# Performance work log

Measured on AMD Instinct MI355X. Metric: run time of the kernel, lower is better.

## Reference

```python
import jax, jax.numpy as jnp
import numpy as np

N_NODES = 100000
N_EDGES = 1600000
D = 64


def setup_inputs() -> dict:
    key = jax.random.key(0)
    k1, k2, k3, k4 = jax.random.split(key, 4)
    x = jax.random.normal(k1, (N_NODES, D), dtype=jnp.float32)
    # glorot-uniform scale for Linear weight [out_dim, in_dim]
    stdv = np.sqrt(6.0 / (D + D)).astype(np.float32)
    W = jax.random.uniform(k2, (D, D), dtype=jnp.float32, minval=-stdv, maxval=stdv)
    bias = jnp.zeros((D,), dtype=jnp.float32)  # forward() uses a zero bias
    edge_index = jax.random.randint(k3, (2, N_EDGES), 0, N_NODES, dtype=jnp.int64)
    counts = jax.random.randint(k4, (N_NODES,), 0, 16, dtype=jnp.int64)
    out_edge_index = jnp.arange(N_EDGES, dtype=jnp.int64)
    return {"x": x, "W": W, "bias": bias, "edge_index": edge_index,
            "counts": counts, "out_edge_index": out_edge_index, "layer_i": 0}


def reference(x, W, bias, edge_index, counts, out_edge_index, layer_i):
    # GCN layer: y = x @ W^T; gather by source; scatter-sum by destination; add bias.
    # counts / out_edge_index / layer_i are layout hints for the fused CUDA kernel
    # (mygraph.gcn) and do not change the math.
    y = x @ W.T                              # [N, D_out]
    src = edge_index[0]                      # [E]
    dst = edge_index[1]                      # [E]
    msgs = y[src]                            # [E, D_out] edge gather
    out = jax.ops.segment_sum(msgs, dst, num_segments=x.shape[0])  # [N, D_out]
    return out + bias
```

## Files before the change

### kernel.cpp

```cpp
#include <hip/hip_runtime.h>


#define DIM 64
#define BN 64
#define BN_SHIFT 6
#define BN_MASK 63
#define NB_MAX 2048
#define PB 256
#define KMAX 8
#define CAPE 1536
#define OVF_MAX 262144
#define AGS 72

typedef __attribute__((ext_vector_type(8))) short short8;
typedef __attribute__((ext_vector_type(4))) float f32x4;

__device__ __forceinline__ unsigned short f32_to_bf16_rne(float f) {
    unsigned u = __float_as_uint(f);
    unsigned r = u + 0x7FFFu + ((u >> 16) & 1u);
    return (unsigned short)(r >> 16);
}

__device__ __forceinline__ void pk2(float a, float b, unsigned &ph, unsigned &pl) {
    unsigned ha = f32_to_bf16_rne(a);
    unsigned hb = f32_to_bf16_rne(b);
    ph = ha | (hb << 16);
    float fa = __uint_as_float(ha << 16);
    float fb = __uint_as_float(hb << 16);
    unsigned la = f32_to_bf16_rne(a - fa);
    unsigned lb = f32_to_bf16_rne(b - fb);
    pl = la | (lb << 16);
}

__device__ __forceinline__ f32x4 mfma16(uint4 a, uint4 b, f32x4 c) {
    return __builtin_amdgcn_mfma_f32_16x16x32_bf16(
        __builtin_bit_cast(short8, a), __builtin_bit_cast(short8, b), c, 0, 0, 0);
}

__global__ __launch_bounds__(1024) void fused_prep_reg_kernel(
        const float* __restrict__ x, const int* __restrict__ ei,
        ushort4* __restrict__ xb4, int* __restrict__ gcnt,
        int* __restrict__ binned, int* __restrict__ ovf,
        int* __restrict__ ovfcnt, int E, int N, int nb, int total4) {
    __shared__ int h[NB_MAX];
    const int t = threadIdx.x;
    const int bid = blockIdx.x;

    for (int b = t; b < nb; b += 1024) h[b] = 0;
    __syncthreads();

    int es[KMAX], ds[KMAX];
    #pragma unroll
    for (int k = 0; k < KMAX; ++k) {
        int e = (k * PB + bid) * 1024 + t;
        if (e < E) {
            es[k] = ei[e];
            ds[k] = ei[E + e];
            atomicAdd(&h[ds[k] >> BN_SHIFT], 1);
        } else {
            ds[k] = -1;
        }
    }

    for (int i = bid * 1024 + t; i < total4; i += PB * 1024) {
        float4 v = ((const float4*)x)[i];
        ushort4 o;
        o.x = f32_to_bf16_rne(v.x); o.y = f32_to_bf16_rne(v.y);
        o.z = f32_to_bf16_rne(v.z); o.w = f32_to_bf16_rne(v.w);
        xb4[i] = o;
    }
    if (bid == 0 && t < 16) {
        ushort4 z; z.x = 0; z.y = 0; z.z = 0; z.w = 0;
        xb4[(size_t)N * 16 + t] = z;
    }
    __syncthreads();

    for (int b = t; b < nb; b += 1024) {
        int c = h[b];
        int base = (c > 0) ? atomicAdd(&gcnt[b], c) : 0;
        h[b] = b * CAPE + base;
    }
    __syncthreads();

    #pragma unroll
    for (int k = 0; k < KMAX; ++k) {
        if (ds[k] >= 0) {
            int b = ds[k] >> BN_SHIFT;
            int p = atomicAdd(&h[b], 1);
            if (p < b * CAPE + CAPE) {
                binned[p] = (es[k] << BN_SHIFT) | (ds[k] & BN_MASK);
            } else {
                int q = atomicAdd(ovfcnt, 1);
                if (q < OVF_MAX) { ovf[2 * q] = es[k]; ovf[2 * q + 1] = ds[k]; }
            }
        }
    }
}

__global__ __launch_bounds__(1024) void fused_prep_kernel(
        const float* __restrict__ x, const int* __restrict__ ei,
        ushort4* __restrict__ xb4, int* __restrict__ gcnt,
        int* __restrict__ binned, int* __restrict__ ovf,
        int* __restrict__ ovfcnt, int E, int N, int nb, int total4) {
    __shared__ int h[NB_MAX];
    const int t = threadIdx.x;
    const int bid = blockIdx.x;

    for (int b = t; b < nb; b += 1024) h[b] = 0;
    __syncthreads();

    for (int i = bid * 1024 + t; i < total4; i += PB * 1024) {
        float4 v = ((const float4*)x)[i];
        ushort4 o;
        o.x = f32_to_bf16_rne(v.x); o.y = f32_to_bf16_rne(v.y);
        o.z = f32_to_bf16_rne(v.z); o.w = f32_to_bf16_rne(v.w);
        xb4[i] = o;
    }
    if (bid == 0 && t < 16) {
        ushort4 z; z.x = 0; z.y = 0; z.z = 0; z.w = 0;
        xb4[(size_t)N * 16 + t] = z;
    }

    for (int e = bid * 1024 + t; e < E; e += PB * 1024)
        atomicAdd(&h[ei[E + e] >> BN_SHIFT], 1);
    __syncthreads();

    for (int b = t; b < nb; b += 1024) {
        int c = h[b];
        int base = (c > 0) ? atomicAdd(&gcnt[b], c) : 0;
        h[b] = b * CAPE + base;
    }
    __syncthreads();

    for (int e = bid * 1024 + t; e < E; e += PB * 1024) {
        int s = ei[e];
        int d = ei[E + e];
        int b = d >> BN_SHIFT;
        int p = atomicAdd(&h[b], 1);
        if (p < b * CAPE + CAPE) {
            binned[p] = (s << BN_SHIFT) | (d & BN_MASK);
        } else {
            int q = atomicAdd(ovfcnt, 1);
            if (q < OVF_MAX) { ovf[2 * q] = s; ovf[2 * q + 1] = d; }
        }
    }
}

__device__ __forceinline__ void acc8(float (&a)[8], const uint4& v) {
    a[0] += __uint_as_float(v.x << 16); a[1] += __uint_as_float(v.x & 0xFFFF0000u);
    a[2] += __uint_as_float(v.y << 16); a[3] += __uint_as_float(v.y & 0xFFFF0000u);
    a[4] += __uint_as_float(v.z << 16); a[5] += __uint_as_float(v.z & 0xFFFF0000u);
    a[6] += __uint_as_float(v.w << 16); a[7] += __uint_as_float(v.w & 0xFFFF0000u);
}

#define PACK_STORE(AR, ROW)                                                   \
    do {                                                                      \
        unsigned ph0, ph1, ph2, ph3, pl0, pl1, pl2, pl3;                      \
        pk2(AR[0], AR[1], ph0, pl0); pk2(AR[2], AR[3], ph1, pl1);             \
        pk2(AR[4], AR[5], ph2, pl2); pk2(AR[6], AR[7], ph3, pl3);             \
        const int dco = (lane & 7) << 3;                                      \
        if (lane < 8) {                                                       \
            uint4 v; v.x = ph0; v.y = ph1; v.z = ph2; v.w = ph3;              \
            *(uint4*)&aggh[(ROW) * AGS + dco] = v;                            \
        } else if (lane < 16) {                                               \
            uint4 v; v.x = pl0; v.y = pl1; v.z = pl2; v.w = pl3;              \
            *(uint4*)&aggl[(ROW) * AGS + dco] = v;                            \
        }                                                                     \
    } while (0)

__global__ __launch_bounds__(256) void sort_gather_kernel(
        const unsigned short* __restrict__ xh, const float* __restrict__ xf,
        const int* __restrict__ binned, const int* __restrict__ gcnt,
        const int* __restrict__ ovf, const int* __restrict__ ovfcnt,
        const float* __restrict__ W, const float* __restrict__ bias,
        float* __restrict__ out, int N) {
    __shared__ int cnt[BN];
    __shared__ int basel[BN + 1];
    __shared__ int tmp[BN];
    __shared__ int slds[CAPE];
    __shared__ __align__(16) unsigned short aggh[BN * AGS];
    __shared__ __align__(16) unsigned short aggl[BN * AGS];

    const int t = threadIdx.x;
    const int g = blockIdx.x;
    const int lane = t & 63;
    const int wid = t >> 6;
    const int node0 = g << BN_SHIFT;

    const int seg0 = g * CAPE;
    int len = gcnt[g];
    if (len > CAPE) len = CAPE;
    const int seg1 = seg0 + len;

    if (t < BN) cnt[t] = 0;
    __syncthreads();

    for (int i = seg0 + t; i < seg1; i += 256)
        atomicAdd(&cnt[binned[i] & BN_MASK], 1);
    __syncthreads();

    int myv = (t < BN) ? cnt[t] : 0;
    if (t < BN) tmp[t] = myv;
    __syncthreads();
    #pragma unroll
    for (int d = 1; d < BN; d <<= 1) {
        int u = (t < BN && t >= d) ? tmp[t - d] : 0;
        __syncthreads();
        if (t < BN) tmp[t] += u;
        __syncthreads();
    }
    if (t < BN) basel[t] = tmp[t] - myv;
    if (t == BN - 1) basel[BN] = tmp[t];
    if (t < BN) cnt[t] = tmp[t] - myv;
    __syncthreads();

    for (int i = seg0 + t; i < seg1; i += 256) {
        int v = binned[i];
        int p = atomicAdd(&cnt[v & BN_MASK], 1);
        slds[p] = v >> BN_SHIFT;
    }
    __syncthreads();

    const int sub8 = lane >> 3;
    const int fb   = (lane & 7) << 3;
    const int zrow = N;
    for (int q = wid; q < (BN >> 2); q += 4) {
        const int nl = q << 2;
        int b0 = basel[nl + 0], e0 = basel[nl + 1];
        int b1 = basel[nl + 1], e1 = basel[nl + 2];
        int b2 = basel[nl + 2], e2 = basel[nl + 3];
        int b3 = basel[nl + 3], e3 = basel[nl + 4];
        int c0 = (e0 - b0 + 7) >> 3, c1 = (e1 - b1 + 7) >> 3;
        int c2 = (e2 - b2 + 7) >> 3, c3 = (e3 - b3 + 7) >> 3;
        int cmax = max(max(c0, c1), max(c2, c3));
        cmax = __builtin_amdgcn_readfirstlane(cmax);

        float A0[8] = {0.f,0.f,0.f,0.f,0.f,0.f,0.f,0.f};
        float A1[8] = {0.f,0.f,0.f,0.f,0.f,0.f,0.f,0.f};
        float A2[8] = {0.f,0.f,0.f,0.f,0.f,0.f,0.f,0.f};
        float A3[8] = {0.f,0.f,0.f,0.f,0.f,0.f,0.f,0.f};

        for (int c = 0; c < cmax; ++c) {
            const int o = (c << 3) + sub8;
            int i0 = b0 + o, i1 = b1 + o, i2 = b2 + o, i3 = b3 + o;
            int s0 = slds[min(i0, CAPE - 1)];
            int s1 = slds[min(i1, CAPE - 1)];
            int s2 = slds[min(i2, CAPE - 1)];
            int s3 = slds[min(i3, CAPE - 1)];
            s0 = (i0 < e0) ? s0 : zrow;
            s1 = (i1 < e1) ? s1 : zrow;
            s2 = (i2 < e2) ? s2 : zrow;
            s3 = (i3 < e3) ? s3 : zrow;
            uint4 v0 = *(const uint4*)(xh + (size_t)s0 * DIM + fb);
            uint4 v1 = *(const uint4*)(xh + (size_t)s1 * DIM + fb);
            uint4 v2 = *(const uint4*)(xh + (size_t)s2 * DIM + fb);
            uint4 v3 = *(const uint4*)(xh + (size_t)s3 * DIM + fb);
            acc8(A0, v0); acc8(A1, v1); acc8(A2, v2); acc8(A3, v3);
        }

        #pragma unroll
        for (int d = 8; d <= 32; d <<= 1) {
            #pragma unroll
            for (int j = 0; j < 8; ++j) {
                A0[j] += __shfl_xor(A0[j], d, 64);
                A1[j] += __shfl_xor(A1[j], d, 64);
                A2[j] += __shfl_xor(A2[j], d, 64);
                A3[j] += __shfl_xor(A3[j], d, 64);
            }
        }

        PACK_STORE(A0, nl + 0);
        PACK_STORE(A1, nl + 1);
        PACK_STORE(A2, nl + 2);
        PACK_STORE(A3, nl + 3);
    }

    __syncthreads();

    {
        const int mbase = wid << 4;
        const int l15 = lane & 15;
        const int kq  = lane >> 4;

        const unsigned short* arow_h = aggh + (mbase + l15) * AGS + (kq << 3);
        const unsigned short* arow_l = aggl + (mbase + l15) * AGS + (kq << 3);
        uint4 ah0 = *(const uint4*)(arow_h);
        uint4 ah1 = *(const uint4*)(arow_h + 32);
        uint4 al0 = *(const uint4*)(arow_l);
        uint4 al1 = *(const uint4*)(arow_l + 32);

        f32x4 acc[4];
        #pragma unroll
        for (int n = 0; n < 4; ++n) {
            float bb = bias[(n << 4) + l15];
            acc[n] = (f32x4){bb, bb, bb, bb};
        }

        #pragma unroll
        for (int n = 0; n < 4; ++n) {
            const float* wr = W + (size_t)((n << 4) + l15) * DIM + (kq << 3);
            float4 wa = *(const float4*)(wr);
            float4 wb = *(const float4*)(wr + 4);
            float4 wc = *(const float4*)(wr + 32);
            float4 wd = *(const float4*)(wr + 36);
            uint4 bh0, bl0, bh1, bl1;
            pk2(wa.x, wa.y, bh0.x, bl0.x); pk2(wa.z, wa.w, bh0.y, bl0.y);
            pk2(wb.x, wb.y, bh0.z, bl0.z); pk2(wb.z, wb.w, bh0.w, bl0.w);
            pk2(wc.x, wc.y, bh1.x, bl1.x); pk2(wc.z, wc.w, bh1.y, bl1.y);
            pk2(wd.x, wd.y, bh1.z, bl1.z); pk2(wd.z, wd.w, bh1.w, bl1.w);
            acc[n] = mfma16(ah0, bh0, acc[n]);
            acc[n] = mfma16(al0, bh0, acc[n]);
            acc[n] = mfma16(ah0, bl0, acc[n]);
            acc[n] = mfma16(ah1, bh1, acc[n]);
            acc[n] = mfma16(al1, bh1, acc[n]);
            acc[n] = mfma16(ah1, bl1, acc[n]);
        }

        #pragma unroll
        for (int n = 0; n < 4; ++n) {
            #pragma unroll
            for (int i = 0; i < 4; ++i) {
                int node = node0 + mbase + (kq << 2) + i;
                if (node < N)
                    out[(size_t)node * DIM + (n << 4) + l15] = acc[n][i];
            }
        }
    }

    __syncthreads();
    int oc = *ovfcnt;
    if (oc > 0) {
        if (oc > OVF_MAX) oc = OVF_MAX;
        for (int i = wid; i < oc; i += 4) {
            int s = ovf[2 * i];
            int d = ovf[2 * i + 1];
            if ((d >> BN_SHIFT) == g) {
                float v = xf[(size_t)s * DIM + lane];
                float rr0 = 0.f, rr1 = 0.f, rr2 = 0.f, rr3 = 0.f;
                #pragma unroll
                for (int k = 0; k < DIM; k += 4) {
                    rr0 += __int_as_float(__builtin_amdgcn_readlane(__float_as_int(v), k + 0)) * W[(size_t)lane * DIM + k + 0];
                    rr1 += __int_as_float(__builtin_amdgcn_readlane(__float_as_int(v), k + 1)) * W[(size_t)lane * DIM + k + 1];
                    rr2 += __int_as_float(__builtin_amdgcn_readlane(__float_as_int(v), k + 2)) * W[(size_t)lane * DIM + k + 2];
                    rr3 += __int_as_float(__builtin_amdgcn_readlane(__float_as_int(v), k + 3)) * W[(size_t)lane * DIM + k + 3];
                }
                atomicAdd(&out[(size_t)d * DIM + lane], (rr0 + rr1) + (rr2 + rr3));
            }
        }
    }
}

__global__ void gcn_scatter_kernel(const float* __restrict__ x,
                                   const int* __restrict__ edge_index,
                                   float* __restrict__ out, int n_edges) {
    int gid = blockIdx.x * blockDim.x + threadIdx.x;
    int e = gid >> 4;
    if (e >= n_edges) return;
    int j = (gid & 15) << 2;
    int src = edge_index[e];
    int dst = edge_index[n_edges + e];
    const float4 v = *(const float4*)(x + (size_t)src * DIM + j);
    float* o = out + (size_t)dst * DIM + j;
    atomicAdd(o + 0, v.x); atomicAdd(o + 1, v.y);
    atomicAdd(o + 2, v.z); atomicAdd(o + 3, v.w);
}

__global__ void gcn_linear_inplace_kernel(float* __restrict__ out,
                                          const float* __restrict__ W,
                                          const float* __restrict__ bias,
                                          int n_nodes) {
    __shared__ float Wt[DIM * DIM];
    __shared__ float rows[4][DIM];
    int tid = threadIdx.x;
    int col = tid & 63;
    int r = tid >> 6;
    for (int i = tid; i < DIM * DIM; i += 256) {
        int c = i >> 6, k = i & 63;
        Wt[k * DIM + c] = W[i];
    }
    int row = blockIdx.x * 4 + r;
    if (row < n_nodes) rows[r][col] = out[(size_t)row * DIM + col];
    __syncthreads();
    if (row < n_nodes) {
        float a = 0.f;
        #pragma unroll
        for (int k = 0; k < DIM; ++k) a += rows[r][k] * Wt[k * DIM + col];
        out[(size_t)row * DIM + col] = a + bias[col];
    }
}

extern "C" void kernel_launch(void* const* d_in, const int* in_sizes, int n_in,
                              void* d_out, int out_size, void* d_ws, size_t ws_size,
                              hipStream_t stream) {
    const float* x          = (const float*)d_in[0];
    const float* W          = (const float*)d_in[1];
    const float* bias       = (const float*)d_in[2];
    const int*   edge_index = (const int*)d_in[3];

    const int E = in_sizes[3] / 2;
    const int N = in_sizes[0] / DIM;
    float* out = (float*)d_out;

    const int nb = (N + BN - 1) >> BN_SHIFT;

    auto align256 = [](size_t v) { return (v + 255) & ~(size_t)255; };
    const size_t xb_b   = align256(((size_t)N + 1) * DIM * 2);
    const size_t bin_b  = align256((size_t)nb * CAPE * 4);
    const size_t cnt_b  = align256(((size_t)nb + 64) * 4);
    const size_t ovf_b  = align256((size_t)OVF_MAX * 2 * 4);
    const size_t needA = xb_b + bin_b + cnt_b + ovf_b;

    if (nb <= NB_MAX && N < (1 << 24) && ws_size >= needA) {
        char* p = (char*)d_ws;
        ushort4* xb4 = (ushort4*)p;          p += xb_b;
        int* binned  = (int*)p;              p += bin_b;
        int* gcnt    = (int*)p;              p += cnt_b;
        int* ovf     = (int*)p;
        int* ovfcnt  = gcnt + nb;

        const int total4 = N * DIM / 4;

        hipMemsetAsync(gcnt, 0, cnt_b, stream);
        if ((long long)E <= (long long)PB * 1024 * KMAX) {
            fused_prep_reg_kernel<<<PB, 1024, 0, stream>>>(
                x, edge_index, xb4, gcnt, binned, ovf, ovfcnt, E, N, nb, total4);
        } else {
            fused_prep_kernel<<<PB, 1024, 0, stream>>>(
                x, edge_index, xb4, gcnt, binned, ovf, ovfcnt, E, N, nb, total4);
        }
        sort_gather_kernel<<<nb, 256, 0, stream>>>(
            (const unsigned short*)xb4, x, binned, gcnt, ovf, ovfcnt,
            W, bias, out, N);
    } else {
        hipMemsetAsync(d_out, 0, (size_t)out_size * sizeof(float), stream);
        long long total = (long long)E * 16;
        int grid = (int)((total + 255) / 256);
        gcn_scatter_kernel<<<grid, 256, 0, stream>>>(x, edge_index, out, E);
        int lgrid = (N + 3) / 4;
        gcn_linear_inplace_kernel<<<lgrid, 256, 0, stream>>>(out, W, bias, N);
    }
}
```

Baseline: 175.6 us.

## Use 512-thread blocks for sort_gather and a wave-shuffle prefix scan

Doubles the sort_gather block to 512 threads (8 waves), so the edge histogram, the scatter into LDS and the per-node gather loop are split across twice as many waves. Only the first 4 waves run the MFMA linear stage. The 64-entry exclusive prefix scan now uses __shfl_up inside a single wave instead of a barrier-heavy LDS scan, which removes many __syncthreads. The cost is more idle waves during the MFMA phase and launch bounds that ask for 8 waves per SIMD, which may cap register use.

After: 215.2 us. 22.5% more time.

```diff
diff --git a/kernel.cpp b/kernel.cpp
--- a/kernel.cpp
+++ b/kernel.cpp
@@ -11,6 +11,7 @@
 #define CAPE 1536
 #define OVF_MAX 262144
 #define AGS 72
+#define SGT 512
 
 typedef __attribute__((ext_vector_type(8))) short short8;
 typedef __attribute__((ext_vector_type(4))) float f32x4;
@@ -168,7 +169,7 @@
         }                                                                     \
     } while (0)
 
-__global__ __launch_bounds__(256) void sort_gather_kernel(
+__global__ __launch_bounds__(SGT, 8) void sort_gather_kernel(
         const unsigned short* __restrict__ xh, const float* __restrict__ xf,
         const int* __restrict__ binned, const int* __restrict__ gcnt,
         const int* __restrict__ ovf, const int* __restrict__ ovfcnt,
@@ -176,7 +177,6 @@
         float* __restrict__ out, int N) {
     __shared__ int cnt[BN];
     __shared__ int basel[BN + 1];
-    __shared__ int tmp[BN];
     __shared__ int slds[CAPE];
     __shared__ __align__(16) unsigned short aggh[BN * AGS];
     __shared__ __align__(16) unsigned short aggl[BN * AGS];
@@ -195,26 +195,25 @@
     if (t < BN) cnt[t] = 0;
     __syncthreads();
 
-    for (int i = seg0 + t; i < seg1; i += 256)
+    for (int i = seg0 + t; i < seg1; i += SGT)
         atomicAdd(&cnt[binned[i] & BN_MASK], 1);
     __syncthreads();
 
-    int myv = (t < BN) ? cnt[t] : 0;
-    if (t < BN) tmp[t] = myv;
-    __syncthreads();
-    #pragma unroll
-    for (int d = 1; d < BN; d <<= 1) {
-        int u = (t < BN && t >= d) ? tmp[t - d] : 0;
-        __syncthreads();
-        if (t < BN) tmp[t] += u;
-        __syncthreads();
-    }
-    if (t < BN) basel[t] = tmp[t] - myv;
-    if (t == BN - 1) basel[BN] = tmp[t];
-    if (t < BN) cnt[t] = tmp[t] - myv;
-    __syncthreads();
-
-    for (int i = seg0 + t; i < seg1; i += 256) {
+    if (t < BN) {
+        int myv = cnt[t];
+        int v = myv;
+        #pragma unroll
+        for (int d = 1; d < BN; d <<= 1) {
+            int u = __shfl_up(v, d, 64);
+            if (t >= d) v += u;
+        }
+        basel[t] = v - myv;
+        if (t == BN - 1) basel[BN] = v;
+        cnt[t] = v - myv;
+    }
+    __syncthreads();
+
+    for (int i = seg0 + t; i < seg1; i += SGT) {
         int v = binned[i];
         int p = atomicAdd(&cnt[v & BN_MASK], 1);
         slds[p] = v >> BN_SHIFT;
@@ -224,7 +223,7 @@
     const int sub8 = lane >> 3;
     const int fb   = (lane & 7) << 3;
     const int zrow = N;
-    for (int q = wid; q < (BN >> 2); q += 4) {
+    for (int q = wid; q < (BN >> 2); q += 8) {
         const int nl = q << 2;
         int b0 = basel[nl + 0], e0 = basel[nl + 1];
         int b1 = basel[nl + 1], e1 = basel[nl + 2];
@@ -277,7 +276,7 @@
 
     __syncthreads();
 
-    {
+    if (wid < 4) {
         const int mbase = wid << 4;
         const int l15 = lane & 15;
         const int kq  = lane >> 4;
@@ -331,7 +330,7 @@
     int oc = *ovfcnt;
     if (oc > 0) {
         if (oc > OVF_MAX) oc = OVF_MAX;
-        for (int i = wid; i < oc; i += 4) {
+        for (int i = wid; i < oc; i += 8) {
             int s = ovf[2 * i];
             int d = ovf[2 * i + 1];
             if ((d >> BN_SHIFT) == g) {
@@ -428,7 +427,7 @@
             fused_prep_kernel<<<PB, 1024, 0, stream>>>(
                 x, edge_index, xb4, gcnt, binned, ovf, ovfcnt, E, N, nb, total4);
         }
-        sort_gather_kernel<<<nb, 256, 0, stream>>>(
+        sort_gather_kernel<<<nb, SGT, 0, stream>>>(
             (const unsigned short*)xb4, x, binned, gcnt, ovf, ovfcnt,
             W, bias, out, N);
     } else {
```

## Sub-sort edges by source tile within each destination and use a wave-shuffle scan

Applied to the files above, without the earlier changes.

The in-block counting sort now bins edges by (destination node, source tile), with 16 coarse source tiles, instead of by destination alone. This orders each node's gathers by source address, so concurrently running blocks touch similar regions of the bf16 feature table and should get better L2 and L1 locality. The 64-entry shared-memory scan with repeated barriers is replaced by a 1024-bin scan built from wave shuffles plus a per-wave sum. CAPE shrinks and the LDS row padding (AGS 72 to 64) is removed to cut shared memory use and raise occupancy. Dropping the padding risks LDS bank conflicts on the aggregation tiles, and the smaller CAPE pushes more edges into the overflow path when bins are full.

Result: no change. 174.6 us (-0.6%).

```diff
diff --git a/kernel.cpp b/kernel.cpp
--- a/kernel.cpp
+++ b/kernel.cpp
@@ -8,9 +8,10 @@
 #define NB_MAX 2048
 #define PB 256
 #define KMAX 8
-#define CAPE 1536
+#define CAPE 1280
 #define OVF_MAX 262144
-#define AGS 72
+#define AGS 64
+#define NBIN 1024
 
 typedef __attribute__((ext_vector_type(8))) short short8;
 typedef __attribute__((ext_vector_type(4))) float f32x4;
@@ -173,10 +174,10 @@
         const int* __restrict__ binned, const int* __restrict__ gcnt,
         const int* __restrict__ ovf, const int* __restrict__ ovfcnt,
         const float* __restrict__ W, const float* __restrict__ bias,
-        float* __restrict__ out, int N) {
-    __shared__ int cnt[BN];
+        float* __restrict__ out, int N, int shift) {
+    __shared__ int cnt[NBIN];
     __shared__ int basel[BN + 1];
-    __shared__ int tmp[BN];
+    __shared__ int wsum[4];
     __shared__ int slds[CAPE];
     __shared__ __align__(16) unsigned short aggh[BN * AGS];
     __shared__ __align__(16) unsigned short aggl[BN * AGS];
@@ -192,32 +193,48 @@
     if (len > CAPE) len = CAPE;
     const int seg1 = seg0 + len;
 
-    if (t < BN) cnt[t] = 0;
-    __syncthreads();
-
-    for (int i = seg0 + t; i < seg1; i += 256)
-        atomicAdd(&cnt[binned[i] & BN_MASK], 1);
-    __syncthreads();
-
-    int myv = (t < BN) ? cnt[t] : 0;
-    if (t < BN) tmp[t] = myv;
-    __syncthreads();
-    #pragma unroll
-    for (int d = 1; d < BN; d <<= 1) {
-        int u = (t < BN && t >= d) ? tmp[t - d] : 0;
-        __syncthreads();
-        if (t < BN) tmp[t] += u;
-        __syncthreads();
-    }
-    if (t < BN) basel[t] = tmp[t] - myv;
-    if (t == BN - 1) basel[BN] = tmp[t];
-    if (t < BN) cnt[t] = tmp[t] - myv;
+    for (int i = t; i < NBIN; i += 256) cnt[i] = 0;
     __syncthreads();
 
     for (int i = seg0 + t; i < seg1; i += 256) {
         int v = binned[i];
-        int p = atomicAdd(&cnt[v & BN_MASK], 1);
-        slds[p] = v >> BN_SHIFT;
+        int tile = min(15, (v >> BN_SHIFT) >> shift);
+        atomicAdd(&cnt[((v & BN_MASK) << 4) | tile], 1);
+    }
+    __syncthreads();
+
+    {
+        int c0 = cnt[4 * t + 0], c1 = cnt[4 * t + 1];
+        int c2 = cnt[4 * t + 2], c3 = cnt[4 * t + 3];
+        int s = c0 + c1 + c2 + c3;
+        int incl = s;
+        #pragma unroll
+        for (int d = 1; d < 64; d <<= 1) {
+            int u = __shfl_up(incl, d, 64);
+            if (lane >= d) incl += u;
+        }
+        if (lane == 63) wsum[wid] = incl;
+        __syncthreads();
+        int woff = 0;
+        for (int w = 0; w < wid; ++w) woff += wsum[w];
+        int excl = woff + incl - s;
+        cnt[4 * t + 0] = excl;
+        cnt[4 * t + 1] = excl + c0;
+        cnt[4 * t + 2] = excl + c0 + c1;
+        cnt[4 * t + 3] = excl + c0 + c1 + c2;
+    }
+    __syncthreads();
+
+    if (t < BN) basel[t] = cnt[t << 4];
+    if (t == 0) basel[BN] = len;
+    __syncthreads();
+
+    for (int i = seg0 + t; i < seg1; i += 256) {
+        int v = binned[i];
+        int src = v >> BN_SHIFT;
+        int tile = min(15, src >> shift);
+        int p = atomicAdd(&cnt[((v & BN_MASK) << 4) | tile], 1);
+        slds[p] = src;
     }
     __syncthreads();
 
@@ -403,6 +420,9 @@
 
     const int nb = (N + BN - 1) >> BN_SHIFT;
 
+    int shift = 0;
+    while (((long long)(N - 1) >> shift) > 15) ++shift;
+
     auto align256 = [](size_t v) { return (v + 255) & ~(size_t)255; };
     const size_t xb_b   = align256(((size_t)N + 1) * DIM * 2);
     const size_t bin_b  = align256((size_t)nb * CAPE * 4);
@@ -430,7 +450,7 @@
         }
         sort_gather_kernel<<<nb, 256, 0, stream>>>(
             (const unsigned short*)xb4, x, binned, gcnt, ovf, ovfcnt,
-            W, bias, out, N);
+            W, bias, out, N, shift);
     } else {
         hipMemsetAsync(d_out, 0, (size_t)out_size * sizeof(float), stream);
         long long total = (long long)E * 16;
```
